# Optimization experiments

Measured on AMD Instinct MI355X. Metric: run time of the kernel, lower is better.

## Reference

```python
import jax, jax.numpy as jnp
import numpy as np

N_NODES = 100000
N_EDGES = 1600000
D_IN, D_HID, D_OUT = 64, 64, 32


def _glorot(key, shape):
    fan_in = shape[0]
    return jax.random.normal(key, shape, dtype=jnp.float32) / np.sqrt(fan_in)


def setup_inputs() -> dict:
    key = jax.random.key(0)
    ks = jax.random.split(key, 12)
    x = jax.random.normal(ks[0], (N_NODES, D_IN), dtype=jnp.float32)
    edge_index = jax.random.randint(ks[1], (2, N_EDGES), 0, N_NODES, dtype=jnp.int32)
    dims = [(D_IN, D_HID), (D_HID, D_HID), (D_HID, D_OUT)]
    params = {}
    for i, (din, dout) in enumerate(dims):
        params[f"Wl{i}"] = _glorot(ks[2 + 3 * i], (din, dout))
        params[f"Wr{i}"] = _glorot(ks[3 + 3 * i], (din, dout))
        params[f"b{i}"] = jnp.zeros((dout,), dtype=jnp.float32)
    return {"x": x, "edge_index": edge_index, **params}


def _sage_conv(h, src, dst, deg_inv, Wl, Wr, b):
    # mean-aggregate neighbor features: gather from src, scatter-sum to dst
    msg_sum = jax.ops.segment_sum(h[src], dst, num_segments=N_NODES)  # [N, F]
    mean = msg_sum * deg_inv[:, None]
    # lin_l(mean) + bias + lin_r(h)  (PyG SAGEConv: bias lives in lin_l)
    return mean @ Wl + b + h @ Wr


def reference(x, edge_index, Wl0, Wr0, b0, Wl1, Wr1, b1, Wl2, Wr2, b2):
    src, dst = edge_index[0], edge_index[1]
    deg = jax.ops.segment_sum(jnp.ones((N_EDGES,), x.dtype), dst, num_segments=N_NODES)
    deg_inv = 1.0 / jnp.maximum(deg, 1.0)  # mean with clamp for isolated nodes
    h = jax.nn.elu(_sage_conv(x, src, dst, deg_inv, Wl0, Wr0, b0))
    h = jax.nn.elu(_sage_conv(h, src, dst, deg_inv, Wl1, Wr1, b1))
    return _sage_conv(h, src, dst, deg_inv, Wl2, Wr2, b2)
```

## Files before the change

### kernel.cpp

```cpp
#include <hip/hip_runtime.h>
#include <cstdint>
#include <cstddef>


constexpr int SBW = 256;
constexpr int LOGSBW = 8;
constexpr int CAPS = 4608;
constexpr int CAPSP = 5632;
constexpr int CHK = 2048;

typedef __attribute__((ext_vector_type(8))) short s16x8;
typedef __attribute__((ext_vector_type(4))) float f32x4;
typedef __attribute__((ext_vector_type(2))) float f32x2;

__device__ inline unsigned short f2bf(float f) {
  unsigned u = __builtin_bit_cast(unsigned, f);
  u += 0x7FFFu + ((u >> 16) & 1u);
  return (unsigned short)(u >> 16);
}
__device__ inline float bf2f(unsigned short b) {
  unsigned u = ((unsigned)b) << 16;
  return __builtin_bit_cast(float, u);
}
__device__ inline unsigned char f2fp8(float f) {
  int p = __builtin_amdgcn_cvt_pk_fp8_f32(f, f, 0, false);
  return (unsigned char)(p & 0xFF);
}


__global__ __launch_bounds__(256) void bin_stage(const int* __restrict__ src,
                                                 const int* __restrict__ dst,
                                                 int* __restrict__ bcur,
                                                 unsigned int* __restrict__ coarse,
                                                 int NSB, int E,
                                                 const float* __restrict__ Wl0,
                                                 const float* __restrict__ Wr0,
                                                 const float* __restrict__ Wl1,
                                                 const float* __restrict__ Wr1,
                                                 const float* __restrict__ Wl2,
                                                 const float* __restrict__ Wr2,
                                                 unsigned short* __restrict__ Wsw) {
  __shared__ int h[512];
  __shared__ unsigned ed[CHK];
  __shared__ short sb[CHK];
  const int tid = threadIdx.x;
  const int bbl = (E + CHK - 1) / CHK;
  if ((int)blockIdx.x >= bbl) {
    int g = (blockIdx.x - bbl) * 256 + tid;
    if (g >= 10240) return;
    int s = g * 2;
    int layer, off;
    if (s < 8192)       { layer = 0; off = 0; }
    else if (s < 16384) { layer = 1; off = 8192; }
    else                { layer = 2; off = 16384; }
    int t = s - off;
    int D = (layer == 2) ? 32 : 64;
    int NTT = D / 16;
    int tt = t >> 10;
    int rem = t & 1023;
    int plane = rem >> 9;
    int rem2 = rem & 511;
    int lane = rem2 >> 3;
    int j = rem2 & 7;
    int q = lane >> 4, m = lane & 15;
    int k = plane * 32 + q * 8 + j;
    const float* W;
    int c;
    if (tt < NTT) {
      c = tt;
      W = (layer == 0) ? Wl0 : (layer == 1) ? Wl1 : Wl2;
    } else {
      c = tt - NTT;
      W = (layer == 0) ? Wr0 : (layer == 1) ? Wr1 : Wr2;
    }
    int col = c * 16 + m;
    unsigned lo = f2bf(W[k * D + col]);
    unsigned hi = f2bf(W[(k + 1) * D + col]);
    *(unsigned*)&Wsw[s] = lo | (hi << 16);
    return;
  }
  for (int i = tid; i < NSB; i += 256) h[i] = 0;
  __syncthreads();
  const int e0 = blockIdx.x * CHK;
  const int e1 = min(E, e0 + CHK);
  for (int e = e0 + tid; e < e1; e += 256) {
    int d = dst[e];
    int s = src[e];
    int b = d >> LOGSBW;
    ed[e - e0] = (unsigned)s | ((unsigned)(d & (SBW - 1)) << 17);
    sb[e - e0] = (short)b;
    atomicAdd(&h[b], 1);
  }
  __syncthreads();
  for (int i = tid; i < NSB; i += 256) {
    int c = h[i];
    h[i] = c ? (i * CAPS + atomicAdd(&bcur[i], c)) : 0;
  }
  __syncthreads();
  const int n = e1 - e0;
  for (int k = tid; k < n; k += 256) {
    int b = sb[k];
    int pos = atomicAdd(&h[b], 1);
    if (pos < (b + 1) * CAPS)
      coarse[pos] = ed[k];
  }
}


__global__ __launch_bounds__(256) void super_csr(const unsigned int* __restrict__ coarse,
                                                 const int* __restrict__ bcur,
                                                 int* __restrict__ rowstart,
                                                 int* __restrict__ degarr,
                                                 float* __restrict__ deg_inv,
                                                 int* __restrict__ colidx,
                                                 int N) {
  __shared__ int cnt[SBW];
  __shared__ int sc[SBW];
  __shared__ int cur[SBW];
  const int b = blockIdx.x;
  const int tid = threadIdx.x;
  cnt[tid] = 0;
  __syncthreads();
  const int ec = min(bcur[b], CAPS);
  const int baseC = b * CAPS;
  const int baseP = b * CAPSP;
  for (int e = tid; e < ec; e += 256)
    atomicAdd(&cnt[coarse[baseC + e] >> 17], 1);
  __syncthreads();
  int v = cnt[tid];
  int pc = (v + 7) & ~7;
  sc[tid] = pc;
  __syncthreads();
  for (int off = 1; off < SBW; off <<= 1) {
    int y = sc[tid];
    if (tid >= off) y += sc[tid - off];
    __syncthreads();
    sc[tid] = y;
    __syncthreads();
  }
  int pex = sc[tid] - pc;
  cur[tid] = pex;
  int gn = b * SBW + tid;
  if (gn < N) {
    rowstart[gn] = baseP + pex;
    degarr[gn] = pc;
    deg_inv[gn] = 1.0f / (float)(v > 1 ? v : 1);
  }
  __syncthreads();
  for (int e = tid; e < ec; e += 256) {
    unsigned p = coarse[baseC + e];
    int dl = (int)(p >> 17);
    int s = (int)(p & 0x1FFFFu);
    int l = atomicAdd(&cur[dl], 1);
    if (l < CAPSP)
      colidx[baseP + l] = s;
  }
  int pe = pex + pc;
  if (pe > CAPSP) pe = CAPSP;
  for (int l = pex + v; l < pe; ++l) colidx[baseP + l] = N;
}


__global__ __launch_bounds__(256) void gemm0_mfma(const float* __restrict__ x,
                                                  const unsigned short* __restrict__ Wf,
                                                  const float* __restrict__ bias,
                                                  unsigned char* __restrict__ t_out,
                                                  unsigned short* __restrict__ r_out,
                                                  int N) {
  constexpr int DOUT = 64;
  constexpr int NTT = 4;
  const int tid = threadIdx.x;
  if (blockIdx.x == 0 && tid < 16)
    ((unsigned*)t_out)[(size_t)N * 16 + tid] = 0u;
  const int wv = tid >> 6, lane = tid & 63;
  const int q = lane >> 4, m = lane & 15;
  const int row = blockIdx.x * 64 + wv * 16 + m;
  const int rowc = row < N ? row : N - 1;
  const float* xp = &x[(size_t)rowc * 64];
  float4 f0 = *(const float4*)&xp[q * 8];
  float4 f1 = *(const float4*)&xp[q * 8 + 4];
  float4 f2 = *(const float4*)&xp[32 + q * 8];
  float4 f3 = *(const float4*)&xp[32 + q * 8 + 4];
  s16x8 a0, a1;
  a0[0] = (short)f2bf(f0.x); a0[1] = (short)f2bf(f0.y);
  a0[2] = (short)f2bf(f0.z); a0[3] = (short)f2bf(f0.w);
  a0[4] = (short)f2bf(f1.x); a0[5] = (short)f2bf(f1.y);
  a0[6] = (short)f2bf(f1.z); a0[7] = (short)f2bf(f1.w);
  a1[0] = (short)f2bf(f2.x); a1[1] = (short)f2bf(f2.y);
  a1[2] = (short)f2bf(f2.z); a1[3] = (short)f2bf(f2.w);
  a1[4] = (short)f2bf(f3.x); a1[5] = (short)f2bf(f3.y);
  a1[6] = (short)f2bf(f3.z); a1[7] = (short)f2bf(f3.w);

  f32x4 acc[2 * NTT];
#pragma unroll
  for (int c = 0; c < 2 * NTT; ++c) acc[c] = (f32x4){0.f, 0.f, 0.f, 0.f};
#pragma unroll
  for (int c = 0; c < 2 * NTT; ++c) {
    s16x8 b0 = *(const s16x8*)&Wf[(c * 2 + 0) * 512 + lane * 8];
    s16x8 b1 = *(const s16x8*)&Wf[(c * 2 + 1) * 512 + lane * 8];
    acc[c] = __builtin_amdgcn_mfma_f32_16x16x32_bf16(a0, b0, acc[c], 0, 0, 0);
    acc[c] = __builtin_amdgcn_mfma_f32_16x16x32_bf16(a1, b1, acc[c], 0, 0, 0);
  }

  const int orow = blockIdx.x * 64 + wv * 16 + q * 4;
#pragma unroll
  for (int c = 0; c < NTT; ++c) {
#pragma unroll
    for (int i = 0; i < 4; ++i) {
      int r_ = orow + i;
      if (r_ < N) t_out[(size_t)r_ * DOUT + c * 16 + m] = f2fp8(acc[c][i]);
    }
  }
#pragma unroll
  for (int c = 0; c < NTT; ++c) {
    float bv = bias[c * 16 + m];
#pragma unroll
    for (int i = 0; i < 4; ++i) {
      int r_ = orow + i;
      if (r_ < N) r_out[(size_t)r_ * DOUT + c * 16 + m] = f2bf(acc[NTT + c][i] + bv);
    }
  }
}


template <int DOUT, bool TFP8, bool RB16>
__global__ __launch_bounds__(256) void gemm_mfma(const unsigned short* __restrict__ Hm,
                                                 const unsigned short* __restrict__ Wf,
                                                 const float* __restrict__ bias,
                                                 void* __restrict__ t_out,
                                                 void* __restrict__ r_out, int N) {
  constexpr int NTT = DOUT / 16;
  constexpr int ROWB = TFP8 ? DOUT : DOUT * 2;
  const int tid = threadIdx.x;
  if (blockIdx.x == 0 && tid < ROWB / 4)
    ((unsigned*)((char*)t_out + (size_t)N * ROWB))[tid] = 0u;
  const int wv = tid >> 6, lane = tid & 63;
  const int q = lane >> 4, m = lane & 15;
  const int row = blockIdx.x * 64 + wv * 16 + m;
  const int rowc = row < N ? row : N - 1;
  const s16x8 a0 = *(const s16x8*)&Hm[(size_t)rowc * 64 + q * 8];
  const s16x8 a1 = *(const s16x8*)&Hm[(size_t)rowc * 64 + 32 + q * 8];

  f32x4 acc[2 * NTT];
#pragma unroll
  for (int c = 0; c < 2 * NTT; ++c) acc[c] = (f32x4){0.f, 0.f, 0.f, 0.f};
#pragma unroll
  for (int c = 0; c < 2 * NTT; ++c) {
    s16x8 b0 = *(const s16x8*)&Wf[(c * 2 + 0) * 512 + lane * 8];
    s16x8 b1 = *(const s16x8*)&Wf[(c * 2 + 1) * 512 + lane * 8];
    acc[c] = __builtin_amdgcn_mfma_f32_16x16x32_bf16(a0, b0, acc[c], 0, 0, 0);
    acc[c] = __builtin_amdgcn_mfma_f32_16x16x32_bf16(a1, b1, acc[c], 0, 0, 0);
  }

  const int orow = blockIdx.x * 64 + wv * 16 + q * 4;
#pragma unroll
  for (int c = 0; c < NTT; ++c) {
#pragma unroll
    for (int i = 0; i < 4; ++i) {
      int r_ = orow + i;
      if (r_ < N) {
        if (TFP8)
          ((unsigned char*)t_out)[(size_t)r_ * DOUT + c * 16 + m] = f2fp8(acc[c][i]);
        else
          ((unsigned short*)t_out)[(size_t)r_ * DOUT + c * 16 + m] = f2bf(acc[c][i]);
      }
    }
  }
#pragma unroll
  for (int c = 0; c < NTT; ++c) {
    float bv = bias[c * 16 + m];
#pragma unroll
    for (int i = 0; i < 4; ++i) {
      int r_ = orow + i;
      if (r_ < N) {
        if (RB16)
          ((unsigned short*)r_out)[(size_t)r_ * DOUT + c * 16 + m] =
              f2bf(acc[NTT + c][i] + bv);
        else
          ((float*)r_out)[(size_t)r_ * DOUT + c * 16 + m] = acc[NTT + c][i] + bv;
      }
    }
  }
}


__global__ __launch_bounds__(256) void gather_fp8(const uint2* __restrict__ t,
                                                  const unsigned short* __restrict__ r,
                                                  const float* __restrict__ deg_inv,
                                                  const int* __restrict__ rowstart,
                                                  const int* __restrict__ degarr,
                                                  const int* __restrict__ colidx,
                                                  unsigned short* __restrict__ Xout,
                                                  int N) {
  int node = blockIdx.x * 32 + (threadIdx.x >> 3);
  int lane = threadIdx.x & 7;
  if (node >= N) return;
  int b = rowstart[node];
  int e = b + degarr[node];
  float s[8];
#pragma unroll
  for (int k = 0; k < 8; ++k) s[k] = 0.f;
  for (int i = b; i < e; i += 8) {
    int4 c0 = *(const int4*)&colidx[i];
    int4 c1 = *(const int4*)&colidx[i + 4];
    uint2 v[8];
    v[0] = t[(size_t)c0.x * 8 + lane];
    v[1] = t[(size_t)c0.y * 8 + lane];
    v[2] = t[(size_t)c0.z * 8 + lane];
    v[3] = t[(size_t)c0.w * 8 + lane];
    v[4] = t[(size_t)c1.x * 8 + lane];
    v[5] = t[(size_t)c1.y * 8 + lane];
    v[6] = t[(size_t)c1.z * 8 + lane];
    v[7] = t[(size_t)c1.w * 8 + lane];
#pragma unroll
    for (int j = 0; j < 8; ++j) {
      f32x2 p0 = __builtin_amdgcn_cvt_pk_f32_fp8((int)v[j].x, false);
      f32x2 p1 = __builtin_amdgcn_cvt_pk_f32_fp8((int)v[j].x, true);
      f32x2 p2 = __builtin_amdgcn_cvt_pk_f32_fp8((int)v[j].y, false);
      f32x2 p3 = __builtin_amdgcn_cvt_pk_f32_fp8((int)v[j].y, true);
      s[0] += p0[0]; s[1] += p0[1]; s[2] += p1[0]; s[3] += p1[1];
      s[4] += p2[0]; s[5] += p2[1]; s[6] += p3[0]; s[7] += p3[1];
    }
  }
  float dv = deg_inv[node];
  const s16x8 rv = *(const s16x8*)&r[(size_t)node * 64 + lane * 8];
  float a[8];
#pragma unroll
  for (int k = 0; k < 8; ++k) a[k] = s[k] * dv + bf2f((unsigned short)rv[k]);
  s16x8 hv;
#pragma unroll
  for (int k = 0; k < 8; ++k) {
    float ak = a[k] > 0.f ? a[k] : (expf(a[k]) - 1.f);
    hv[k] = (short)f2bf(ak);
  }
  *(s16x8*)&Xout[(size_t)node * 64 + lane * 8] = hv;
}


__global__ __launch_bounds__(256) void gather_out(const uint2* __restrict__ t,
                                                  const float* __restrict__ r,
                                                  const float* __restrict__ deg_inv,
                                                  const int* __restrict__ rowstart,
                                                  const int* __restrict__ degarr,
                                                  const int* __restrict__ colidx,
                                                  float* __restrict__ out, int N) {
  constexpr int L = 8;
  int node = blockIdx.x * 32 + threadIdx.x / L;
  int lane = threadIdx.x & (L - 1);
  if (node >= N) return;
  int b = rowstart[node];
  int e = b + degarr[node];
  float s0 = 0.f, s1 = 0.f, s2 = 0.f, s3 = 0.f;
  for (int i = b; i < e; i += 8) {
    int4 c0 = *(const int4*)&colidx[i];
    int4 c1 = *(const int4*)&colidx[i + 4];
    uint2 v[8];
    v[0] = t[(size_t)c0.x * L + lane];
    v[1] = t[(size_t)c0.y * L + lane];
    v[2] = t[(size_t)c0.z * L + lane];
    v[3] = t[(size_t)c0.w * L + lane];
    v[4] = t[(size_t)c1.x * L + lane];
    v[5] = t[(size_t)c1.y * L + lane];
    v[6] = t[(size_t)c1.z * L + lane];
    v[7] = t[(size_t)c1.w * L + lane];
#pragma unroll
    for (int j = 0; j < 8; ++j) {
      s0 += bf2f((unsigned short)(v[j].x & 0xFFFFu));
      s1 += bf2f((unsigned short)(v[j].x >> 16));
      s2 += bf2f((unsigned short)(v[j].y & 0xFFFFu));
      s3 += bf2f((unsigned short)(v[j].y >> 16));
    }
  }
  float dv = deg_inv[node];
  float4 rv = *(const float4*)&r[(size_t)node * 32 + 4 * lane];
  *(float4*)&out[(size_t)node * 32 + 4 * lane] =
      make_float4(s0 * dv + rv.x, s1 * dv + rv.y, s2 * dv + rv.z, s3 * dv + rv.w);
}


extern "C" void kernel_launch(void* const* d_in, const int* in_sizes, int n_in,
                              void* d_out, int out_size, void* d_ws, size_t ws_size,
                              hipStream_t stream) {
  const float* x   = (const float*)d_in[0];
  const int*   ei  = (const int*)d_in[1];
  const float* Wl0 = (const float*)d_in[2];
  const float* Wr0 = (const float*)d_in[3];
  const float* b0  = (const float*)d_in[4];
  const float* Wl1 = (const float*)d_in[5];
  const float* Wr1 = (const float*)d_in[6];
  const float* b1  = (const float*)d_in[7];
  const float* Wl2 = (const float*)d_in[8];
  const float* Wr2 = (const float*)d_in[9];
  const float* b2  = (const float*)d_in[10];
  float* out = (float*)d_out;

  const int N = in_sizes[0] / 64;
  const int E = in_sizes[1] / 2;
  const int* srcv = ei;
  const int* dstv = ei + E;
  const int NSB = (N + SBW - 1) >> LOGSBW;

  auto al = [](size_t v) { return (v + 255) & ~(size_t)255; };
  char* w = (char*)d_ws;
  size_t oBcur = 0;
  size_t oRow  = oBcur + al(4 * (size_t)NSB);
  size_t oDeg  = oRow + al(4 * (size_t)N);
  size_t oDinv = oDeg + al(4 * (size_t)N);
  size_t oWsw  = oDinv + al(4 * (size_t)N);
  size_t oBin  = oWsw + al(2 * 20480);
  size_t oCol  = oBin + al(4 * (size_t)NSB * CAPS);
  size_t oP8   = oCol + al(4 * (size_t)NSB * CAPSP);
  size_t oP16  = oP8 + al((size_t)(N + 1) * 64);
  size_t oX    = oP16 + al((size_t)(N + 1) * 64);
  size_t oR    = oX + al(2 * (size_t)N * 64);

  int*            bcur     = (int*)(w + oBcur);
  int*            rowstart = (int*)(w + oRow);
  int*            degarr   = (int*)(w + oDeg);
  float*          deg_inv  = (float*)(w + oDinv);
  unsigned short* Wsw      = (unsigned short*)(w + oWsw);
  unsigned*       coarse   = (unsigned*)(w + oBin);
  int*            colidx   = (int*)(w + oCol);
  unsigned char*  P8       = (unsigned char*)(w + oP8);
  unsigned short* P16      = (unsigned short*)(w + oP16);
  unsigned short* X        = (unsigned short*)(w + oX);
  unsigned short* Rb       = (unsigned short*)(w + oR);
  float*          Rf       = (float*)(w + oR);

  hipMemsetAsync(bcur, 0, (size_t)NSB * 4, stream);

  int bbl = (E + CHK - 1) / CHK;
  bin_stage<<<bbl + 40, 256, 0, stream>>>(srcv, dstv, bcur, coarse, NSB, E,
                                          Wl0, Wr0, Wl1, Wr1, Wl2, Wr2, Wsw);
  super_csr<<<NSB, 256, 0, stream>>>(coarse, bcur, rowstart, degarr, deg_inv, colidx, N);

  int gb = (N + 63) / 64;
  int ggb = (N + 31) / 32;
  gemm0_mfma<<<gb, 256, 0, stream>>>(x, Wsw, b0, P8, Rb, N);
  gather_fp8<<<ggb, 256, 0, stream>>>((const uint2*)P8, Rb, deg_inv, rowstart,
                                      degarr, colidx, X, N);
  gemm_mfma<64, true, true><<<gb, 256, 0, stream>>>(X, Wsw + 8192, b1, P8, Rb, N);
  gather_fp8<<<ggb, 256, 0, stream>>>((const uint2*)P8, Rb, deg_inv, rowstart,
                                      degarr, colidx, X, N);
  gemm_mfma<32, false, false><<<gb, 256, 0, stream>>>(X, Wsw + 16384, b2, P16, Rf, N);
  gather_out<<<ggb, 256, 0, stream>>>((const uint2*)P16, Rf, deg_inv, rowstart,
                                      degarr, colidx, out, N);
}
```

Baseline: 254.6 us.

## Fuse CSR build with first GEMM, replace memset with init kernel, pad rows to 4

The memset and weight swizzle move into a small init kernel, and binning becomes its own kernel. The per-superblock CSR build and the layer-0 GEMM now run as one launch, with separate block ranges doing each job, so they can overlap. Row padding drops from multiples of 8 to multiples of 4, and the gather loops gain a 4-wide tail, so fewer padding sentinel gathers are issued. The trade-off is an extra kernel launch for the init step and a bit more code in the gather tails.

Result: faster. 242.7 us (-4.7%).

```diff
diff --git a/kernel.cpp b/kernel.cpp
--- a/kernel.cpp
+++ b/kernel.cpp
@@ -28,57 +28,62 @@
 }
 
 
-__global__ __launch_bounds__(256) void bin_stage(const int* __restrict__ src,
-                                                 const int* __restrict__ dst,
-                                                 int* __restrict__ bcur,
-                                                 unsigned int* __restrict__ coarse,
-                                                 int NSB, int E,
-                                                 const float* __restrict__ Wl0,
-                                                 const float* __restrict__ Wr0,
-                                                 const float* __restrict__ Wl1,
-                                                 const float* __restrict__ Wr1,
-                                                 const float* __restrict__ Wl2,
-                                                 const float* __restrict__ Wr2,
-                                                 unsigned short* __restrict__ Wsw) {
+__global__ __launch_bounds__(256) void init_ws(int* __restrict__ bcur, int NSB,
+                                               const float* __restrict__ Wl0,
+                                               const float* __restrict__ Wr0,
+                                               const float* __restrict__ Wl1,
+                                               const float* __restrict__ Wr1,
+                                               const float* __restrict__ Wl2,
+                                               const float* __restrict__ Wr2,
+                                               unsigned short* __restrict__ Wsw) {
+  const int tid = threadIdx.x;
+  if (blockIdx.x == 0) {
+    for (int i = tid; i < NSB; i += 256) bcur[i] = 0;
+    return;
+  }
+  int g = (blockIdx.x - 1) * 256 + tid;
+  if (g >= 10240) return;
+  int s = g * 2;
+  int layer, off;
+  if (s < 8192)       { layer = 0; off = 0; }
+  else if (s < 16384) { layer = 1; off = 8192; }
+  else                { layer = 2; off = 16384; }
+  int t = s - off;
+  int D = (layer == 2) ? 32 : 64;
+  int NTT = D / 16;
+  int tt = t >> 10;
+  int rem = t & 1023;
+  int plane = rem >> 9;
+  int rem2 = rem & 511;
+  int lane = rem2 >> 3;
+  int j = rem2 & 7;
+  int q = lane >> 4, m = lane & 15;
+  int k = plane * 32 + q * 8 + j;
+  const float* W;
+  int c;
+  if (tt < NTT) {
+    c = tt;
+    W = (layer == 0) ? Wl0 : (layer == 1) ? Wl1 : Wl2;
+  } else {
+    c = tt - NTT;
+    W = (layer == 0) ? Wr0 : (layer == 1) ? Wr1 : Wr2;
+  }
+  int col = c * 16 + m;
+  unsigned lo = f2bf(W[k * D + col]);
+  unsigned hi = f2bf(W[(k + 1) * D + col]);
+  *(unsigned*)&Wsw[s] = lo | (hi << 16);
+}
+
+
+__global__ __launch_bounds__(256) void bin_coarse(const int* __restrict__ src,
+                                                  const int* __restrict__ dst,
+                                                  int* __restrict__ bcur,
+                                                  unsigned int* __restrict__ coarse,
+                                                  int NSB, int E) {
   __shared__ int h[512];
   __shared__ unsigned ed[CHK];
   __shared__ short sb[CHK];
   const int tid = threadIdx.x;
-  const int bbl = (E + CHK - 1) / CHK;
-  if ((int)blockIdx.x >= bbl) {
-    int g = (blockIdx.x - bbl) * 256 + tid;
-    if (g >= 10240) return;
-    int s = g * 2;
-    int layer, off;
-    if (s < 8192)       { layer = 0; off = 0; }
-    else if (s < 16384) { layer = 1; off = 8192; }
-    else                { layer = 2; off = 16384; }
-    int t = s - off;
-    int D = (layer == 2) ? 32 : 64;
-    int NTT = D / 16;
-    int tt = t >> 10;
-    int rem = t & 1023;
-    int plane = rem >> 9;
-    int rem2 = rem & 511;
-    int lane = rem2 >> 3;
-    int j = rem2 & 7;
-    int q = lane >> 4, m = lane & 15;
-    int k = plane * 32 + q * 8 + j;
-    const float* W;
-    int c;
-    if (tt < NTT) {
-      c = tt;
-      W = (layer == 0) ? Wl0 : (layer == 1) ? Wl1 : Wl2;
-    } else {
-      c = tt - NTT;
-      W = (layer == 0) ? Wr0 : (layer == 1) ? Wr1 : Wr2;
-    }
-    int col = c * 16 + m;
-    unsigned lo = f2bf(W[k * D + col]);
-    unsigned hi = f2bf(W[(k + 1) * D + col]);
-    *(unsigned*)&Wsw[s] = lo | (hi << 16);
-    return;
-  }
   for (int i = tid; i < NSB; i += 256) h[i] = 0;
   __syncthreads();
   const int e0 = blockIdx.x * CHK;
@@ -107,74 +112,73 @@
 }
 
 
-__global__ __launch_bounds__(256) void super_csr(const unsigned int* __restrict__ coarse,
+__global__ __launch_bounds__(256) void csr_gemm0(const unsigned int* __restrict__ coarse,
                                                  const int* __restrict__ bcur,
                                                  int* __restrict__ rowstart,
                                                  int* __restrict__ degarr,
                                                  float* __restrict__ deg_inv,
                                                  int* __restrict__ colidx,
-                                                 int N) {
+                                                 const float* __restrict__ x,
+                                                 const unsigned short* __restrict__ Wf,
+                                                 const float* __restrict__ bias,
+                                                 unsigned char* __restrict__ t_out,
+                                                 unsigned short* __restrict__ r_out,
+                                                 int N, int NSB) {
   __shared__ int cnt[SBW];
   __shared__ int sc[SBW];
   __shared__ int cur[SBW];
-  const int b = blockIdx.x;
   const int tid = threadIdx.x;
-  cnt[tid] = 0;
-  __syncthreads();
-  const int ec = min(bcur[b], CAPS);
-  const int baseC = b * CAPS;
-  const int baseP = b * CAPSP;
-  for (int e = tid; e < ec; e += 256)
-    atomicAdd(&cnt[coarse[baseC + e] >> 17], 1);
-  __syncthreads();
-  int v = cnt[tid];
-  int pc = (v + 7) & ~7;
-  sc[tid] = pc;
-  __syncthreads();
-  for (int off = 1; off < SBW; off <<= 1) {
-    int y = sc[tid];
-    if (tid >= off) y += sc[tid - off];
+  if ((int)blockIdx.x < NSB) {
+    const int b = blockIdx.x;
+    cnt[tid] = 0;
     __syncthreads();
-    sc[tid] = y;
+    const int ec = min(bcur[b], CAPS);
+    const int baseC = b * CAPS;
+    const int baseP = b * CAPSP;
+    for (int e = tid; e < ec; e += 256)
+      atomicAdd(&cnt[coarse[baseC + e] >> 17], 1);
     __syncthreads();
-  }
-  int pex = sc[tid] - pc;
-  cur[tid] = pex;
-  int gn = b * SBW + tid;
-  if (gn < N) {
-    rowstart[gn] = baseP + pex;
-    degarr[gn] = pc;
-    deg_inv[gn] = 1.0f / (float)(v > 1 ? v : 1);
-  }
-  __syncthreads();
-  for (int e = tid; e < ec; e += 256) {
-    unsigned p = coarse[baseC + e];
-    int dl = (int)(p >> 17);
-    int s = (int)(p & 0x1FFFFu);
-    int l = atomicAdd(&cur[dl], 1);
-    if (l < CAPSP)
-      colidx[baseP + l] = s;
-  }
-  int pe = pex + pc;
-  if (pe > CAPSP) pe = CAPSP;
-  for (int l = pex + v; l < pe; ++l) colidx[baseP + l] = N;
-}
-
-
-__global__ __launch_bounds__(256) void gemm0_mfma(const float* __restrict__ x,
-                                                  const unsigned short* __restrict__ Wf,
-                                                  const float* __restrict__ bias,
-                                                  unsigned char* __restrict__ t_out,
-                                                  unsigned short* __restrict__ r_out,
-                                                  int N) {
+    int v = cnt[tid];
+    int pc = (v + 3) & ~3;
+    sc[tid] = pc;
+    __syncthreads();
+    for (int off = 1; off < SBW; off <<= 1) {
+      int y = sc[tid];
+      if (tid >= off) y += sc[tid - off];
+      __syncthreads();
+      sc[tid] = y;
+      __syncthreads();
+    }
+    int pex = sc[tid] - pc;
+    cur[tid] = pex;
+    int gn = b * SBW + tid;
+    if (gn < N) {
+      rowstart[gn] = baseP + pex;
+      degarr[gn] = pc;
+      deg_inv[gn] = 1.0f / (float)(v > 1 ? v : 1);
+    }
+    __syncthreads();
+    for (int e = tid; e < ec; e += 256) {
+      unsigned p = coarse[baseC + e];
+      int dl = (int)(p >> 17);
+      int s = (int)(p & 0x1FFFFu);
+      int l = atomicAdd(&cur[dl], 1);
+      if (l < CAPSP)
+        colidx[baseP + l] = s;
+    }
+    int pe = pex + pc;
+    if (pe > CAPSP) pe = CAPSP;
+    for (int l = pex + v; l < pe; ++l) colidx[baseP + l] = N;
+    return;
+  }
   constexpr int DOUT = 64;
   constexpr int NTT = 4;
-  const int tid = threadIdx.x;
-  if (blockIdx.x == 0 && tid < 16)
+  const int gbid = blockIdx.x - NSB;
+  if (gbid == 0 && tid < 16)
     ((unsigned*)t_out)[(size_t)N * 16 + tid] = 0u;
   const int wv = tid >> 6, lane = tid & 63;
   const int q = lane >> 4, m = lane & 15;
-  const int row = blockIdx.x * 64 + wv * 16 + m;
+  const int row = gbid * 64 + wv * 16 + m;
   const int rowc = row < N ? row : N - 1;
   const float* xp = &x[(size_t)rowc * 64];
   float4 f0 = *(const float4*)&xp[q * 8];
@@ -202,7 +206,7 @@
     acc[c] = __builtin_amdgcn_mfma_f32_16x16x32_bf16(a1, b1, acc[c], 0, 0, 0);
   }
 
-  const int orow = blockIdx.x * 64 + wv * 16 + q * 4;
+  const int orow = gbid * 64 + wv * 16 + q * 4;
 #pragma unroll
   for (int c = 0; c < NTT; ++c) {
 #pragma unroll
@@ -300,7 +304,8 @@
   float s[8];
 #pragma unroll
   for (int k = 0; k < 8; ++k) s[k] = 0.f;
-  for (int i = b; i < e; i += 8) {
+  int i = b;
+  for (; i + 8 <= e; i += 8) {
     int4 c0 = *(const int4*)&colidx[i];
     int4 c1 = *(const int4*)&colidx[i + 4];
     uint2 v[8];
@@ -314,6 +319,23 @@
     v[7] = t[(size_t)c1.w * 8 + lane];
 #pragma unroll
     for (int j = 0; j < 8; ++j) {
+      f32x2 p0 = __builtin_amdgcn_cvt_pk_f32_fp8((int)v[j].x, false);
+      f32x2 p1 = __builtin_amdgcn_cvt_pk_f32_fp8((int)v[j].x, true);
+      f32x2 p2 = __builtin_amdgcn_cvt_pk_f32_fp8((int)v[j].y, false);
+      f32x2 p3 = __builtin_amdgcn_cvt_pk_f32_fp8((int)v[j].y, true);
+      s[0] += p0[0]; s[1] += p0[1]; s[2] += p1[0]; s[3] += p1[1];
+      s[4] += p2[0]; s[5] += p2[1]; s[6] += p3[0]; s[7] += p3[1];
+    }
+  }
+  if (i < e) {
+    int4 c0 = *(const int4*)&colidx[i];
+    uint2 v[4];
+    v[0] = t[(size_t)c0.x * 8 + lane];
+    v[1] = t[(size_t)c0.y * 8 + lane];
+    v[2] = t[(size_t)c0.z * 8 + lane];
+    v[3] = t[(size_t)c0.w * 8 + lane];
+#pragma unroll
+    for (int j = 0; j < 4; ++j) {
       f32x2 p0 = __builtin_amdgcn_cvt_pk_f32_fp8((int)v[j].x, false);
       f32x2 p1 = __builtin_amdgcn_cvt_pk_f32_fp8((int)v[j].x, true);
       f32x2 p2 = __builtin_amdgcn_cvt_pk_f32_fp8((int)v[j].y, false);
@@ -351,7 +373,8 @@
   int b = rowstart[node];
   int e = b + degarr[node];
   float s0 = 0.f, s1 = 0.f, s2 = 0.f, s3 = 0.f;
-  for (int i = b; i < e; i += 8) {
+  int i = b;
+  for (; i + 8 <= e; i += 8) {
     int4 c0 = *(const int4*)&colidx[i];
     int4 c1 = *(const int4*)&colidx[i + 4];
     uint2 v[8];
@@ -365,6 +388,21 @@
     v[7] = t[(size_t)c1.w * L + lane];
 #pragma unroll
     for (int j = 0; j < 8; ++j) {
+      s0 += bf2f((unsigned short)(v[j].x & 0xFFFFu));
+      s1 += bf2f((unsigned short)(v[j].x >> 16));
+      s2 += bf2f((unsigned short)(v[j].y & 0xFFFFu));
+      s3 += bf2f((unsigned short)(v[j].y >> 16));
+    }
+  }
+  if (i < e) {
+    int4 c0 = *(const int4*)&colidx[i];
+    uint2 v[4];
+    v[0] = t[(size_t)c0.x * L + lane];
+    v[1] = t[(size_t)c0.y * L + lane];
+    v[2] = t[(size_t)c0.z * L + lane];
+    v[3] = t[(size_t)c0.w * L + lane];
+#pragma unroll
+    for (int j = 0; j < 4; ++j) {
       s0 += bf2f((unsigned short)(v[j].x & 0xFFFFu));
       s1 += bf2f((unsigned short)(v[j].x >> 16));
       s2 += bf2f((unsigned short)(v[j].y & 0xFFFFu));
@@ -427,16 +465,15 @@
   unsigned short* Rb       = (unsigned short*)(w + oR);
   float*          Rf       = (float*)(w + oR);
 
-  hipMemsetAsync(bcur, 0, (size_t)NSB * 4, stream);
-
   int bbl = (E + CHK - 1) / CHK;
-  bin_stage<<<bbl + 40, 256, 0, stream>>>(srcv, dstv, bcur, coarse, NSB, E,
-                                          Wl0, Wr0, Wl1, Wr1, Wl2, Wr2, Wsw);
-  super_csr<<<NSB, 256, 0, stream>>>(coarse, bcur, rowstart, degarr, deg_inv, colidx, N);
-
   int gb = (N + 63) / 64;
   int ggb = (N + 31) / 32;
-  gemm0_mfma<<<gb, 256, 0, stream>>>(x, Wsw, b0, P8, Rb, N);
+
+  init_ws<<<41, 256, 0, stream>>>(bcur, NSB, Wl0, Wr0, Wl1, Wr1, Wl2, Wr2, Wsw);
+  bin_coarse<<<bbl, 256, 0, stream>>>(srcv, dstv, bcur, coarse, NSB, E);
+  csr_gemm0<<<NSB + gb, 256, 0, stream>>>(coarse, bcur, rowstart, degarr,
+                                          deg_inv, colidx, x, Wsw, b0, P8, Rb,
+                                          N, NSB);
   gather_fp8<<<ggb, 256, 0, stream>>>((const uint2*)P8, Rb, deg_inv, rowstart,
                                       degarr, colidx, X, N);
   gemm_mfma<64, true, true><<<gb, 256, 0, stream>>>(X, Wsw + 8192, b1, P8, Rb, N);
```
